# Optimization experiments

Measured on AMD Instinct MI355X. Metric: run time of the kernel, lower is better.

## Reference

```python
import jax, jax.numpy as jnp
import numpy as np
from jax import lax

B, T, S = 64, 4096, 64


def setup_inputs() -> dict:
    key = jax.random.key(0)
    k1, k2, k3 = jax.random.split(key, 3)
    transition_potentials = jax.random.normal(k1, (S, S), dtype=jnp.float32)
    emission_potentials = jax.random.normal(k2, (B, T, S), dtype=jnp.float32)
    seq_lens = jax.random.randint(k3, (B,), 1, T + 1)
    return {
        "transition_potentials": transition_potentials,
        "emission_potentials": emission_potentials,
        "seq_lens": seq_lens,
    }


def reference(transition_potentials, emission_potentials, seq_lens):
    # potential_normalization='none', potential_scale=1.0 -> normalize is identity.
    # HMM forward algorithm: alpha[t] = logsumexp_i(alpha[t-1,i] + A[i,j]) + emis[t]
    alpha0 = emission_potentials[:, 0, :]  # [B,S]

    def step(alpha_prev, emis_t):
        # alpha_prev: [B,S]; emis_t: [B,S]; transition: [S,S]
        alpha_t = jax.nn.logsumexp(
            alpha_prev[:, :, None] + transition_potentials[None, :, :], axis=1
        ) + emis_t
        return alpha_t, alpha_t

    emis_rest = jnp.moveaxis(emission_potentials[:, 1:, :], 1, 0)  # [T-1,B,S]
    _, alphas = lax.scan(step, alpha0, emis_rest)  # [T-1,B,S]
    alpha = jnp.concatenate([alpha0[None], alphas], axis=0)  # [T,B,S]
    alpha = jnp.moveaxis(alpha, 0, 1)  # [B,T,S]
    log_Z = jax.nn.logsumexp(alpha[:, -1, :], axis=-1)  # [B]
    return alpha, log_Z
```

## Files before the change

### kernel.cpp

```cpp
#include <hip/hip_runtime.h>
#include <hip/hip_bf16.h>


#define BB 64
#define TT 4096
#define SS 64
#define C_CH 64
#define LL 64
#define WARM 24

typedef __attribute__((ext_vector_type(8))) short short8;
typedef __attribute__((ext_vector_type(4))) float f32x4;

#define LOG2E 1.44269504088896340736f
#define LN2F  0.69314718055994530942f

__device__ __forceinline__ float fexp2(float x) {
#if __has_builtin(__builtin_amdgcn_exp2f)
    return __builtin_amdgcn_exp2f(x);
#else
    return exp2f(x);
#endif
}
__device__ __forceinline__ float flog2(float x) {
#if __has_builtin(__builtin_amdgcn_logf)
    return __builtin_amdgcn_logf(x);
#else
    return log2f(x);
#endif
}
__device__ __forceinline__ float bpermf(int idx, float v) {
    return __uint_as_float((unsigned)__builtin_amdgcn_ds_bpermute(idx, (int)__float_as_uint(v)));
}
__device__ __forceinline__ int pack_bf16(float x, float y) {
    __hip_bfloat162 h = __float22bfloat162_rn(make_float2(x, y));
    int r; __builtin_memcpy(&r, &h, 4); return r;
}
union PB { int i[4]; short8 v; };

__device__ __forceinline__ void do_step(f32x4 (&al2)[4], const f32x4 (&er)[4],
                                        const short8 (&Af)[4][2],
                                        int idxM, int idx0, int idx1, int q) {
    float M2 = bpermf(idxM, al2[0].x);

    int pkk[4][2];
    #pragma unroll
    for (int jt = 0; jt < 4; ++jt) {
        float ux = fexp2(al2[jt].x - M2);
        float uy = fexp2(al2[jt].y - M2);
        float uz = fexp2(al2[jt].z - M2);
        float uw = fexp2(al2[jt].w - M2);
        pkk[jt][0] = pack_bf16(ux, uy);
        pkk[jt][1] = pack_bf16(uz, uw);
    }

    short8 Bf[2];
    #pragma unroll
    for (int kh = 0; kh < 2; ++kh) {
        PB pb;
        #pragma unroll
        for (int p = 0; p < 4; ++p) {
            int idx = (p >> 1) ? idx1 : idx0;
            int lo = __builtin_amdgcn_ds_bpermute(idx, pkk[2 * kh + 0][p & 1]);
            int hi = __builtin_amdgcn_ds_bpermute(idx, pkk[2 * kh + 1][p & 1]);
            pb.i[p] = (q >= 2) ? hi : lo;
        }
        Bf[kh] = pb.v;
    }

    #pragma unroll
    for (int jt = 0; jt < 4; ++jt) {
        f32x4 d = {0.f, 0.f, 0.f, 0.f};
        d = __builtin_amdgcn_mfma_f32_16x16x32_bf16(Af[jt][0], Bf[0], d, 0, 0, 0);
        d = __builtin_amdgcn_mfma_f32_16x16x32_bf16(Af[jt][1], Bf[1], d, 0, 0, 0);
        al2[jt].x = fmaf(er[jt].x, LOG2E, M2) + flog2(d.x);
        al2[jt].y = fmaf(er[jt].y, LOG2E, M2) + flog2(d.y);
        al2[jt].z = fmaf(er[jt].z, LOG2E, M2) + flog2(d.z);
        al2[jt].w = fmaf(er[jt].w, LOG2E, M2) + flog2(d.w);
    }
}

__device__ __forceinline__ void load_row(f32x4 (&dst)[4],
                                         const float* __restrict__ eb,
                                         int t, int off) {
    const float* p = eb + (t & (TT - 1)) * SS + off;
    #pragma unroll
    for (int jt = 0; jt < 4; ++jt)
        dst[jt] = *(const f32x4*)(p + 16 * jt);
}

__global__ __launch_bounds__(64)
__attribute__((amdgpu_waves_per_eu(1, 1)))
void hmm_phaseA(const float* __restrict__ trans,
                const float* __restrict__ emis,
                float* __restrict__ out,
                float* __restrict__ ws_warm,
                float* __restrict__ ws_bound) {
    const int lane = threadIdx.x;
    const int n = lane & 15, q = lane >> 4;
    const int w = blockIdx.x;
    const int b = w >> 2, cg = w & 3;
    const int c = 16 * cg + n;
    const bool is_c0 = (c == 0);
    const int off = 4 * q;

    short8 Af[4][2];
    #pragma unroll
    for (int jt = 0; jt < 4; ++jt)
        #pragma unroll
        for (int kh = 0; kh < 2; ++kh) {
            PB pb;
            #pragma unroll
            for (int p = 0; p < 4; ++p) {
                float v0 = __expf(trans[(32 * kh + 8 * q + 2 * p    ) * SS + 16 * jt + n]);
                float v1 = __expf(trans[(32 * kh + 8 * q + 2 * p + 1) * SS + 16 * jt + n]);
                pb.i[p] = pack_bf16(v0, v1);
            }
            Af[jt][kh] = pb.v;
        }

    const int idxM = n << 2;
    const int idx0 = ((n + 16 * ((2 * q + 0) & 3)) & 63) << 2;
    const int idx1 = ((n + 16 * ((2 * q + 1) & 3)) & 63) << 2;

    const float* eb = emis + (size_t)b * TT * SS;
    float*       ob = out  + (size_t)b * TT * SS;

    const int t0 = LL * c - (WARM + 1);

    f32x4 al2[4], e0[4], ebuf[4][4];
    load_row(al2, eb, t0, off);
    #pragma unroll
    for (int jt = 0; jt < 4; ++jt) al2[jt] = al2[jt] * LOG2E;
    load_row(e0, eb, 0, off);
    #pragma unroll
    for (int k = 0; k < 4; ++k) load_row(ebuf[k], eb, t0 + 1 + k, off);

    #pragma unroll 1
    for (int g = 0; g < 6; ++g) {
        #pragma unroll
        for (int k = 0; k < 4; ++k) {
            int s = 4 * g + k + 1;
            f32x4 er[4];
            #pragma unroll
            for (int jt = 0; jt < 4; ++jt) er[jt] = ebuf[k][jt];
            load_row(ebuf[k], eb, t0 + s + 4, off);
            do_step(al2, er, Af, idxM, idx0, idx1, q);
        }
    }
    if (lane < 16)
        ws_warm[b * C_CH + 16 * cg + lane] = al2[0].x * LN2F;

    #pragma unroll 1
    for (int g = 0; g < 16; ++g) {
        #pragma unroll
        for (int k = 0; k < 4; ++k) {
            int s = 25 + 4 * g + k;
            f32x4 er[4];
            #pragma unroll
            for (int jt = 0; jt < 4; ++jt) er[jt] = ebuf[k][jt];
            load_row(ebuf[k], eb, t0 + s + 4, off);
            do_step(al2, er, Af, idxM, idx0, idx1, q);
            if (k == 0 && g == 0 && is_c0) {
                #pragma unroll
                for (int jt = 0; jt < 4; ++jt) al2[jt] = e0[jt] * LOG2E;
            }
            float* p = ob + (t0 + s) * SS + off;
            #pragma unroll
            for (int jt = 0; jt < 4; ++jt)
                *(f32x4*)(p + 16 * jt) = al2[jt] * LN2F;
        }
    }
    if (lane < 16)
        ws_bound[b * C_CH + 16 * cg + lane] = al2[0].x * LN2F;
}

__global__ __launch_bounds__(256)
void hmm_phaseC(float* __restrict__ out,
                const float* __restrict__ ws_warm,
                const float* __restrict__ ws_bound) {
    const int b = blockIdx.x, c = blockIdx.y, tid = threadIdx.x;
    __shared__ float sdelta;

    if (tid < 64) {
        float d = 0.f;
        if (tid > 0 && tid < C_CH)
            d = ws_bound[b * C_CH + tid - 1] - ws_warm[b * C_CH + tid];
        #pragma unroll
        for (int off = 1; off < C_CH; off <<= 1) {
            float v = __shfl_up(d, off, 64);
            if (tid >= off) d += v;
        }
        float dc = __shfl(d, c, 64);
        if (tid == 0) sdelta = dc;
    }
    __syncthreads();
    const float delta = sdelta;

    float4* p4 = (float4*)(out + (size_t)b * TT * SS + (size_t)c * LL * SS);
    float4 last;
    #pragma unroll
    for (int i = 0; i < 4; ++i) {
        int idx = tid + 256 * i;
        float4 v = p4[idx];
        v.x += delta; v.y += delta; v.z += delta; v.w += delta;
        p4[idx] = v;
        last = v;
    }

    if (c == C_CH - 1 && tid >= 240) {
        float mx = fmaxf(fmaxf(last.x, last.y), fmaxf(last.z, last.w));
        #pragma unroll
        for (int off = 8; off >= 1; off >>= 1)
            mx = fmaxf(mx, __shfl_xor(mx, off, 64));
        float sv = __expf(last.x - mx) + __expf(last.y - mx)
                 + __expf(last.z - mx) + __expf(last.w - mx);
        #pragma unroll
        for (int off = 8; off >= 1; off >>= 1)
            sv += __shfl_xor(sv, off, 64);
        if (tid == 240)
            out[(size_t)BB * TT * SS + b] = mx + __logf(sv);
    }
}

extern "C" void kernel_launch(void* const* d_in, const int* in_sizes, int n_in,
                              void* d_out, int out_size, void* d_ws, size_t ws_size,
                              hipStream_t stream) {
    const float* trans = (const float*)d_in[0];
    const float* emis  = (const float*)d_in[1];
    float* out = (float*)d_out;

    float* ws_warm  = (float*)d_ws;
    float* ws_bound = ws_warm + BB * C_CH;

    hmm_phaseA<<<dim3(BB * 4), dim3(64), 0, stream>>>(trans, emis, out,
                                                      ws_warm, ws_bound);
    hmm_phaseC<<<dim3(BB, C_CH), dim3(256), 0, stream>>>(out, ws_warm, ws_bound);
}
```

Baseline: 166.0 us.

## Switch to 16x16x16 bf16 MFMA so exp output feeds B operand without permutes

Replaces the 16x16x32 MFMA pair with four 16x16x16 MFMAs per output tile, choosing a K layout where each lane's exponentiated alpha values already sit in the B-operand position. This removes the per-step ds_bpermute shuffles and selects that rebuilt the B fragments. It also computes the next step's max shift right after the first output tile, taking the cross-lane broadcast off the critical path. The trade-off is twice as many, smaller MFMA instructions per step in the serial recurrence.

```diff
diff --git a/kernel.cpp b/kernel.cpp
--- a/kernel.cpp
+++ b/kernel.cpp
@@ -9,7 +9,7 @@
 #define LL 64
 #define WARM 24
 
-typedef __attribute__((ext_vector_type(8))) short short8;
+typedef __attribute__((ext_vector_type(4))) short bh4;
 typedef __attribute__((ext_vector_type(4))) float f32x4;
 
 #define LOG2E 1.44269504088896340736f
@@ -36,48 +36,43 @@
     __hip_bfloat162 h = __float22bfloat162_rn(make_float2(x, y));
     int r; __builtin_memcpy(&r, &h, 4); return r;
 }
-union PB { int i[4]; short8 v; };
-
-__device__ __forceinline__ void do_step(f32x4 (&al2)[4], const f32x4 (&er)[4],
-                                        const short8 (&Af)[4][2],
-                                        int idxM, int idx0, int idx1, int q) {
-    float M2 = bpermf(idxM, al2[0].x);
-
-    int pkk[4][2];
-    #pragma unroll
-    for (int jt = 0; jt < 4; ++jt) {
-        float ux = fexp2(al2[jt].x - M2);
-        float uy = fexp2(al2[jt].y - M2);
-        float uz = fexp2(al2[jt].z - M2);
-        float uw = fexp2(al2[jt].w - M2);
-        pkk[jt][0] = pack_bf16(ux, uy);
-        pkk[jt][1] = pack_bf16(uz, uw);
-    }
-
-    short8 Bf[2];
-    #pragma unroll
-    for (int kh = 0; kh < 2; ++kh) {
-        PB pb;
-        #pragma unroll
-        for (int p = 0; p < 4; ++p) {
-            int idx = (p >> 1) ? idx1 : idx0;
-            int lo = __builtin_amdgcn_ds_bpermute(idx, pkk[2 * kh + 0][p & 1]);
-            int hi = __builtin_amdgcn_ds_bpermute(idx, pkk[2 * kh + 1][p & 1]);
-            pb.i[p] = (q >= 2) ? hi : lo;
-        }
-        Bf[kh] = pb.v;
-    }
-
+union PB2 { int i[2]; bh4 v; };
+
+__device__ __forceinline__ f32x4 mfma16(bh4 a, bh4 b, f32x4 c) {
+#if __has_builtin(__builtin_amdgcn_mfma_f32_16x16x16bf16_1k)
+    return __builtin_amdgcn_mfma_f32_16x16x16bf16_1k(a, b, c, 0, 0, 0);
+#else
+    asm("v_mfma_f32_16x16x16_bf16 %0, %1, %2, %0" : "+v"(c) : "v"(a), "v"(b));
+    return c;
+#endif
+}
+
+__device__ __forceinline__ float do_step(f32x4 (&al2)[4], const f32x4 (&er)[4],
+                                         const bh4 (&Af)[4][4],
+                                         float M2, int idxM) {
+    bh4 Bf[4];
+    #pragma unroll
+    for (int kb = 0; kb < 4; ++kb) {
+        PB2 pb;
+        pb.i[0] = pack_bf16(fexp2(al2[kb].x - M2), fexp2(al2[kb].y - M2));
+        pb.i[1] = pack_bf16(fexp2(al2[kb].z - M2), fexp2(al2[kb].w - M2));
+        Bf[kb] = pb.v;
+    }
+
+    float M2n = 0.f;
     #pragma unroll
     for (int jt = 0; jt < 4; ++jt) {
         f32x4 d = {0.f, 0.f, 0.f, 0.f};
-        d = __builtin_amdgcn_mfma_f32_16x16x32_bf16(Af[jt][0], Bf[0], d, 0, 0, 0);
-        d = __builtin_amdgcn_mfma_f32_16x16x32_bf16(Af[jt][1], Bf[1], d, 0, 0, 0);
+        #pragma unroll
+        for (int kb = 0; kb < 4; ++kb)
+            d = mfma16(Af[jt][kb], Bf[kb], d);
         al2[jt].x = fmaf(er[jt].x, LOG2E, M2) + flog2(d.x);
         al2[jt].y = fmaf(er[jt].y, LOG2E, M2) + flog2(d.y);
         al2[jt].z = fmaf(er[jt].z, LOG2E, M2) + flog2(d.z);
         al2[jt].w = fmaf(er[jt].w, LOG2E, M2) + flog2(d.w);
-    }
+        if (jt == 0) M2n = bpermf(idxM, al2[0].x);
+    }
+    return M2n;
 }
 
 __device__ __forceinline__ void load_row(f32x4 (&dst)[4],
@@ -104,24 +99,22 @@
     const bool is_c0 = (c == 0);
     const int off = 4 * q;
 
-    short8 Af[4][2];
+    bh4 Af[4][4];
     #pragma unroll
     for (int jt = 0; jt < 4; ++jt)
         #pragma unroll
-        for (int kh = 0; kh < 2; ++kh) {
-            PB pb;
-            #pragma unroll
-            for (int p = 0; p < 4; ++p) {
-                float v0 = __expf(trans[(32 * kh + 8 * q + 2 * p    ) * SS + 16 * jt + n]);
-                float v1 = __expf(trans[(32 * kh + 8 * q + 2 * p + 1) * SS + 16 * jt + n]);
-                pb.i[p] = pack_bf16(v0, v1);
-            }
-            Af[jt][kh] = pb.v;
+        for (int kb = 0; kb < 4; ++kb) {
+            float v0 = __expf(trans[(16 * kb + 4 * q + 0) * SS + 16 * jt + n]);
+            float v1 = __expf(trans[(16 * kb + 4 * q + 1) * SS + 16 * jt + n]);
+            float v2 = __expf(trans[(16 * kb + 4 * q + 2) * SS + 16 * jt + n]);
+            float v3 = __expf(trans[(16 * kb + 4 * q + 3) * SS + 16 * jt + n]);
+            PB2 pb;
+            pb.i[0] = pack_bf16(v0, v1);
+            pb.i[1] = pack_bf16(v2, v3);
+            Af[jt][kb] = pb.v;
         }
 
     const int idxM = n << 2;
-    const int idx0 = ((n + 16 * ((2 * q + 0) & 3)) & 63) << 2;
-    const int idx1 = ((n + 16 * ((2 * q + 1) & 3)) & 63) << 2;
 
     const float* eb = emis + (size_t)b * TT * SS;
     float*       ob = out  + (size_t)b * TT * SS;
@@ -135,6 +128,8 @@
     load_row(e0, eb, 0, off);
     #pragma unroll
     for (int k = 0; k < 4; ++k) load_row(ebuf[k], eb, t0 + 1 + k, off);
+
+    float M2 = bpermf(idxM, al2[0].x);
 
     #pragma unroll 1
     for (int g = 0; g < 6; ++g) {
@@ -145,7 +140,7 @@
             #pragma unroll
             for (int jt = 0; jt < 4; ++jt) er[jt] = ebuf[k][jt];
             load_row(ebuf[k], eb, t0 + s + 4, off);
-            do_step(al2, er, Af, idxM, idx0, idx1, q);
+            M2 = do_step(al2, er, Af, M2, idxM);
         }
     }
     if (lane < 16)
@@ -160,10 +155,14 @@
             #pragma unroll
             for (int jt = 0; jt < 4; ++jt) er[jt] = ebuf[k][jt];
             load_row(ebuf[k], eb, t0 + s + 4, off);
-            do_step(al2, er, Af, idxM, idx0, idx1, q);
-            if (k == 0 && g == 0 && is_c0) {
-                #pragma unroll
-                for (int jt = 0; jt < 4; ++jt) al2[jt] = e0[jt] * LOG2E;
+            M2 = do_step(al2, er, Af, M2, idxM);
+            if (k == 0 && g == 0) {
+                if (is_c0) {
+                    #pragma unroll
+                    for (int jt = 0; jt < 4; ++jt) al2[jt] = e0[jt] * LOG2E;
+                }
+                if (cg == 0)
+                    M2 = bpermf(idxM, al2[0].x);
             }
             float* p = ob + (t0 + s) * SS + off;
             #pragma unroll
```

Result: no change. 168.5 us (+1.5%).
